# Kernel tuning notes

Measured on AMD Instinct MI355X. Metric: run time of the kernel, lower is better.

Reference implementation:

```python
import jax, jax.numpy as jnp
import numpy as np
from math import factorial, sqrt

LMAX = 2
SH = (LMAX + 1) ** 2  # 9 real spherical-harmonic components
N_ATOMS = 1000
N_EDGES = 10000
N_BASIS = 128
N_RADIAL = 20


def _cg_complex(l1, m1, l2, m2, l3, m3):
    # Racah formula for complex Clebsch-Gordan <l1 m1 l2 m2 | l3 m3>
    if m3 != m1 + m2 or not (abs(l1 - l2) <= l3 <= l1 + l2):
        return 0.0
    pre = sqrt((2 * l3 + 1) * factorial(l3 + l1 - l2) * factorial(l3 - l1 + l2)
               * factorial(l1 + l2 - l3) / factorial(l1 + l2 + l3 + 1))
    pre *= sqrt(factorial(l3 + m3) * factorial(l3 - m3) * factorial(l1 - m1)
                * factorial(l1 + m1) * factorial(l2 - m2) * factorial(l2 + m2))
    kmin = max(0, l2 - l3 - m1, l1 - l3 + m2)
    kmax = min(l1 + l2 - l3, l1 - m1, l2 + m2)
    s = 0.0
    for k in range(kmin, kmax + 1):
        s += (-1) ** k / (factorial(k) * factorial(l1 + l2 - l3 - k)
                          * factorial(l1 - m1 - k) * factorial(l2 + m2 - k)
                          * factorial(l3 - l2 + m1 + k) * factorial(l3 - l1 - m2 + k))
    return pre * s


def _u_c2r(l):
    # complex -> real spherical-harmonic change of basis, rows real m, cols complex m
    U = np.zeros((2 * l + 1, 2 * l + 1), dtype=np.complex128)
    U[l, l] = 1.0
    for m in range(1, l + 1):
        U[l + m, l + m] = (-1) ** m / np.sqrt(2.0)
        U[l + m, l - m] = 1.0 / np.sqrt(2.0)
        U[l - m, l - m] = 1j / np.sqrt(2.0)
        U[l - m, l + m] = -1j * (-1) ** m / np.sqrt(2.0)
    return U


def _generate_cg_rsh(lmax):
    # real-SH Clebsch-Gordan tensor with parity invariance (odd l1+l2+l3 zeroed)
    S = (lmax + 1) ** 2
    cg = np.zeros((S, S, S))
    for l1 in range(lmax + 1):
        for l2 in range(lmax + 1):
            for l3 in range(lmax + 1):
                if (l1 + l2 + l3) % 2 == 1 or not (abs(l1 - l2) <= l3 <= l1 + l2):
                    continue
                block = np.zeros((2 * l1 + 1, 2 * l2 + 1, 2 * l3 + 1), dtype=np.complex128)
                for m1 in range(-l1, l1 + 1):
                    for m2 in range(-l2, l2 + 1):
                        m3 = m1 + m2
                        if abs(m3) <= l3:
                            block[m1 + l1, m2 + l2, m3 + l3] = _cg_complex(l1, m1, l2, m2, l3, m3)
                rb = np.einsum('abc,ia,jb,kc->ijk', block, _u_c2r(l1), _u_c2r(l2), np.conj(_u_c2r(l3)))
                cg[l1 * l1:(l1 + 1) ** 2, l2 * l2:(l2 + 1) ** 2, l3 * l3:(l3 + 1) ** 2] = np.real(rb)
    cg[np.abs(cg) < 1e-12] = 0.0
    return cg


_CG_T = _generate_cg_rsh(LMAX)
_I1, _I2, _IO = np.nonzero(_CG_T)
CG = jnp.asarray(_CG_T[_I1, _I2, _IO].astype(np.float32))  # [P] nonzero CG values
IDX_IN_1 = jnp.asarray(_I1)
IDX_IN_2 = jnp.asarray(_I2)
IDX_OUT = jnp.asarray(_IO)
_LIDX = np.repeat(np.arange(LMAX + 1), 2 * np.arange(LMAX + 1) + 1)  # degree l per SH index
WIDX = jnp.asarray(_LIDX[_I1])  # filter degree per CG path (schnetpack Widx)


def setup_inputs() -> dict:
    key = jax.random.key(0)
    ks = jax.random.split(key, 7)
    return {
        "x": jax.random.normal(ks[0], (N_ATOMS, SH, N_BASIS), jnp.float32),
        "radial_ij": jax.random.normal(ks[1], (N_EDGES, N_RADIAL), jnp.float32),
        "dir_ij": jax.random.normal(ks[2], (N_EDGES, SH), jnp.float32),
        "cutoff_ij": jax.random.uniform(ks[3], (N_EDGES, 1), jnp.float32),
        "Wf": jax.random.normal(ks[4], (N_RADIAL, (LMAX + 1) * N_BASIS), jnp.float32) * 0.1,
        "bf": jnp.zeros(((LMAX + 1) * N_BASIS,), jnp.float32),
        "idx_i": jax.random.randint(ks[5], (N_EDGES,), 0, N_ATOMS),
        "idx_j": jax.random.randint(ks[6], (N_EDGES,), 0, N_ATOMS),
        "n_atoms": N_ATOMS,
    }


def reference(x, radial_ij, dir_ij, cutoff_ij, Wf, bf, idx_i, idx_j, n_atoms):
    E = radial_ij.shape[0]
    # radial filter: Dense(n_radial -> (lmax+1)*C) * cutoff, gathered per CG path by degree l
    Wij = (radial_ij @ Wf + bf) * cutoff_ij                     # [E,(L+1)*C]
    Wij = Wij.reshape(E, LMAX + 1, N_BASIS)[:, WIDX]            # [E,P,C]
    xj = x[idx_j][:, IDX_IN_2]                                  # gather neighbor feats: [E,P,C]
    v = Wij * dir_ij[:, IDX_IN_1, None] * CG[None, :, None] * xj  # [E,P,C]
    # scatter_add over CG paths -> output SH index
    yij = jnp.zeros((E, SH, N_BASIS), v.dtype).at[:, IDX_OUT, :].add(v)  # [E,S,C]
    # scatter_add over edges -> receiving atom
    y = jax.ops.segment_sum(yij, idx_i, num_segments=n_atoms)   # [n_atoms,S,C]
    return y
```

## Files before the change

### kernel.cpp

```cpp
#include <hip/hip_runtime.h>


#define SH_N 9
#define NB 128
#define NR 20
#define NSUB 2
#define NT (NSUB * NB)
#define CAPL 128

namespace cgc {

struct CD { double re, im; };
constexpr CD cmul(CD x, CD y) { return {x.re * y.re - x.im * y.im, x.re * y.im + x.im * y.re}; }
constexpr CD cadd(CD x, CD y) { return {x.re + y.re, x.im + y.im}; }
constexpr CD cconj(CD x) { return {x.re, -x.im}; }

constexpr double FACT[10] = {1., 1., 2., 6., 24., 120., 720., 5040., 40320., 362880.};

constexpr double csqrt(double a) {
    if (a <= 0.0) return 0.0;
    double x = a < 1.0 ? 1.0 : a;
    for (int i = 0; i < 40; ++i) x = 0.5 * (x + a / x);
    return x;
}

constexpr double cg_complex(int l1, int m1, int l2, int m2, int l3, int m3) {
    if (m3 != m1 + m2) return 0.0;
    int dl = l1 > l2 ? l1 - l2 : l2 - l1;
    if (l3 < dl || l3 > l1 + l2) return 0.0;
    double pre = csqrt((2.0 * l3 + 1.0) * FACT[l3 + l1 - l2] * FACT[l3 - l1 + l2]
                       * FACT[l1 + l2 - l3] / FACT[l1 + l2 + l3 + 1]);
    pre = pre * csqrt(FACT[l3 + m3] * FACT[l3 - m3] * FACT[l1 - m1] * FACT[l1 + m1]
                      * FACT[l2 - m2] * FACT[l2 + m2]);
    int kmin = 0;
    if (l2 - l3 - m1 > kmin) kmin = l2 - l3 - m1;
    if (l1 - l3 + m2 > kmin) kmin = l1 - l3 + m2;
    int kmax = l1 + l2 - l3;
    if (l1 - m1 < kmax) kmax = l1 - m1;
    if (l2 + m2 < kmax) kmax = l2 + m2;
    double s = 0.0;
    for (int k = kmin; k <= kmax; ++k) {
        double term = 1.0 / (FACT[k] * FACT[l1 + l2 - l3 - k] * FACT[l1 - m1 - k]
                             * FACT[l2 + m2 - k] * FACT[l3 - l2 + m1 + k] * FACT[l3 - l1 - m2 + k]);
        s += (k & 1) ? -term : term;
    }
    return pre * s;
}

struct U5 { CD m[5][5]; };
constexpr U5 u_c2r(int l) {
    U5 u{};
    const double isq = csqrt(0.5);
    u.m[l][l] = {1.0, 0.0};
    for (int mm = 1; mm <= l; ++mm) {
        double sgn = (mm & 1) ? -1.0 : 1.0;
        u.m[l + mm][l + mm] = {sgn * isq, 0.0};
        u.m[l + mm][l - mm] = {isq, 0.0};
        u.m[l - mm][l - mm] = {0.0, isq};
        u.m[l - mm][l + mm] = {0.0, -sgn * isq};
    }
    return u;
}

struct CGTab { float v[SH_N][SH_N][SH_N]; };

constexpr CGTab build_cg() {
    CGTab t{};
    for (int l1 = 0; l1 <= 2; ++l1)
    for (int l2 = 0; l2 <= 2; ++l2)
    for (int l3 = 0; l3 <= 2; ++l3) {
        int dl = l1 > l2 ? l1 - l2 : l2 - l1;
        if (((l1 + l2 + l3) & 1) || l3 < dl || l3 > l1 + l2) continue;
        U5 U1 = u_c2r(l1), U2 = u_c2r(l2), U3 = u_c2r(l3);
        const int n1 = 2 * l1 + 1, n2 = 2 * l2 + 1, n3 = 2 * l3 + 1;
        double blk[5][5][5] = {};
        for (int a = 0; a < n1; ++a)
        for (int b = 0; b < n2; ++b) {
            int m1 = a - l1, m2 = b - l2, m3 = m1 + m2;
            if (m3 < -l3 || m3 > l3) continue;
            blk[a][b][m3 + l3] = cg_complex(l1, m1, l2, m2, l3, m3);
        }
        for (int i = 0; i < n1; ++i)
        for (int j = 0; j < n2; ++j)
        for (int k = 0; k < n3; ++k) {
            CD s{0.0, 0.0};
            for (int a = 0; a < n1; ++a) {
                if (U1.m[i][a].re == 0.0 && U1.m[i][a].im == 0.0) continue;
                for (int b = 0; b < n2; ++b) {
                    if (U2.m[j][b].re == 0.0 && U2.m[j][b].im == 0.0) continue;
                    int m3 = (a - l1) + (b - l2);
                    if (m3 < -l3 || m3 > l3) continue;
                    double B = blk[a][b][m3 + l3];
                    if (B == 0.0) continue;
                    CD u3 = cconj(U3.m[k][m3 + l3]);
                    if (u3.re == 0.0 && u3.im == 0.0) continue;
                    CD term = cmul(cmul(U1.m[i][a], U2.m[j][b]), u3);
                    s = cadd(s, CD{term.re * B, term.im * B});
                }
            }
            double v = s.re;
            if (v < 1e-12 && v > -1e-12) v = 0.0;
            t.v[l1 * l1 + i][l2 * l2 + j][l3 * l3 + k] = (float)v;
        }
    }
    return t;
}

}

static constexpr cgc::CGTab CGT = cgc::build_cg();

__device__ __forceinline__ float sel_w(int a, float w0, float w1, float w2) {
    return (a == 0) ? w0 : ((a < 4) ? w1 : w2);
}

__device__ __forceinline__ void comp_edge(
        int e, const float (&xr)[SH_N],
        const float* __restrict__ radial, const float* __restrict__ dir,
        const float* __restrict__ cutoff,
        const float (&wreg)[NR * 3], float b0, float b1, float b2,
        float (&acc)[SH_N]) {
    const float* rad = radial + (size_t)e * NR;
    float a0 = b0, a1 = b1, a2 = b2;
#pragma unroll
    for (int r = 0; r < NR; ++r) {
        const float rv = rad[r];
        a0 = fmaf(rv, wreg[r * 3 + 0], a0);
        a1 = fmaf(rv, wreg[r * 3 + 1], a1);
        a2 = fmaf(rv, wreg[r * 3 + 2], a2);
    }
    const float cut = cutoff[e];
    const float w0 = a0 * cut, w1 = a1 * cut, w2 = a2 * cut;
    const float* dp = dir + (size_t)e * SH_N;
#pragma unroll
    for (int ai = 0; ai < SH_N; ++ai) {
        const float daw = dp[ai] * sel_w(ai, w0, w1, w2);
#pragma unroll
        for (int bi = 0; bi < SH_N; ++bi) {
            const float g = daw * xr[bi];
#pragma unroll
            for (int o = 0; o < SH_N; ++o)
                if (CGT.v[ai][bi][o] != 0.0f)
                    acc[o] = fmaf(CGT.v[ai][bi][o], g, acc[o]);
        }
    }
}

__device__ __forceinline__ void load_xr(float (&xr)[SH_N], int e,
        const float* __restrict__ x, const int* __restrict__ idx_j, int c) {
    const int aj = idx_j[e];
    const float* xp = x + (size_t)aj * (SH_N * NB) + c;
#pragma unroll
    for (int k = 0; k < SH_N; ++k) xr[k] = xp[k * NB];
}


__global__ void __launch_bounds__(NT, 4)
so3_fused_kernel(const float* __restrict__ x,
                 const float* __restrict__ radial,
                 const float* __restrict__ dir,
                 const float* __restrict__ cutoff,
                 const float* __restrict__ Wf,
                 const float* __restrict__ bf,
                 const int* __restrict__ idx_i,
                 const int* __restrict__ idx_j,
                 float* __restrict__ y,
                 int E) {
    const int a    = blockIdx.x;
    const int tid  = threadIdx.x;
    const int sub  = tid >> 7;
    const int c    = tid & (NB - 1);
    const int lane = tid & 63;
    const int wid  = tid >> 6;

    __shared__ int s_list[CAPL];
    __shared__ int s_wsum[NT / 64];
    __shared__ int s_m;

    float wreg[NR * 3];
#pragma unroll
    for (int r = 0; r < NR; ++r)
#pragma unroll
        for (int l = 0; l < 3; ++l)
            wreg[r * 3 + l] = Wf[(r * 3 + l) * NB + c];
    const float b0 = bf[c], b1 = bf[NB + c], b2 = bf[2 * NB + c];

    unsigned long long mask = 0ull;
    int cnt = 0;
    const int E4 = E >> 2;
    const bool fast_scan = (4 * ((E4 + NT - 1) / NT) <= 60);
    if (fast_scan) {
        const int4* p4 = (const int4*)idx_i;
        int b = 0;
        for (int k4 = tid; k4 < E4; k4 += NT, ++b) {
            const int4 q = p4[k4];
            unsigned long long h = (unsigned long long)(q.x == a)
                                 | ((unsigned long long)(q.y == a) << 1)
                                 | ((unsigned long long)(q.z == a) << 2)
                                 | ((unsigned long long)(q.w == a) << 3);
            mask |= h << (4 * b);
        }
        const int kt = 4 * E4 + tid;
        if (tid < (E & 3) && kt < E && idx_i[kt] == a)
            mask |= 1ull << (60 + tid);
        cnt = __popcll(mask);
    } else {
        for (int k = tid; k < E; k += NT) cnt += (idx_i[k] == a);
    }

    int v = cnt;
#pragma unroll
    for (int d = 1; d < 64; d <<= 1) {
        int u = __shfl_up(v, d);
        if (lane >= d) v += u;
    }
    if (lane == 63) s_wsum[wid] = v;
    __syncthreads();
    if (tid == 0) {
        int t = 0;
#pragma unroll
        for (int w = 0; w < NT / 64; ++w) { int q = s_wsum[w]; s_wsum[w] = t; t += q; }
        s_m = t;
    }
    __syncthreads();
    int off = s_wsum[wid] + v - cnt;

    if (fast_scan) {
        unsigned long long mm = mask;
        while (mm) {
            const int p = __ffsll(mm) - 1;
            mm &= mm - 1;
            int k;
            if (p >= 60) k = 4 * E4 + (p - 60);
            else         k = 4 * (tid + (p >> 2) * NT) + (p & 3);
            if (off < CAPL) s_list[off] = k;
            ++off;
        }
    } else if (cnt > 0) {
        for (int k = tid; k < E; k += NT)
            if (idx_i[k] == a) { if (off < CAPL) s_list[off] = k; ++off; }
    }
    __syncthreads();
    const int m = (s_m < CAPL) ? s_m : CAPL;

    float acc[SH_N];
#pragma unroll
    for (int o = 0; o < SH_N; ++o) acc[o] = 0.f;

    int ie = sub;
    if (ie < m) {
        float xrA[SH_N], xrB[SH_N];
        int eA = __builtin_amdgcn_readfirstlane(s_list[ie]);
        load_xr(xrA, eA, x, idx_j, c);
        for (;;) {
            int ien = ie + NSUB;
            if (ien < m) {
                const int eB = __builtin_amdgcn_readfirstlane(s_list[ien]);
                load_xr(xrB, eB, x, idx_j, c);
                comp_edge(eA, xrA, radial, dir, cutoff, wreg, b0, b1, b2, acc);
                ie = ien; ien += NSUB;
                if (ien < m) {
                    eA = __builtin_amdgcn_readfirstlane(s_list[ien]);
                    load_xr(xrA, eA, x, idx_j, c);
                    comp_edge(eB, xrB, radial, dir, cutoff, wreg, b0, b1, b2, acc);
                    ie = ien;
                } else {
                    comp_edge(eB, xrB, radial, dir, cutoff, wreg, b0, b1, b2, acc);
                    break;
                }
            } else {
                comp_edge(eA, xrA, radial, dir, cutoff, wreg, b0, b1, b2, acc);
                break;
            }
        }
    }

    __shared__ float s_red[NSUB][SH_N * NB];
#pragma unroll
    for (int o = 0; o < SH_N; ++o) s_red[sub][o * NB + c] = acc[o];
    __syncthreads();
    float* yo = y + (size_t)a * (SH_N * NB);
    for (int oc = tid; oc < SH_N * NB; oc += NT)
        yo[oc] = s_red[0][oc] + s_red[1][oc];
}


extern "C" void kernel_launch(void* const* d_in, const int* in_sizes, int n_in,
                              void* d_out, int out_size, void* d_ws, size_t ws_size,
                              hipStream_t stream) {
    const float* x      = (const float*)d_in[0];
    const float* radial = (const float*)d_in[1];
    const float* dir    = (const float*)d_in[2];
    const float* cutoff = (const float*)d_in[3];
    const float* Wf     = (const float*)d_in[4];
    const float* bf     = (const float*)d_in[5];
    const int*   idx_i  = (const int*)d_in[6];
    const int*   idx_j  = (const int*)d_in[7];
    float* y = (float*)d_out;
    const int E = in_sizes[6];
    const int n_atoms = out_size / (SH_N * NB);

    so3_fused_kernel<<<n_atoms, NT, 0, stream>>>(x, radial, dir, cutoff, Wf, bf,
                                                 idx_i, idx_j, y, E);
}
```

Before: 26.28 us.

## Split radial filter into separate precompute kernel and widen atom blocks

Moves the per-edge radial dense layer and cutoff multiply into a separate kernel that writes a per-edge, per-channel filter to workspace; the atom kernel then loads these weights instead of holding Wf in registers. Edge parallelism per atom block is doubled to four sub-groups. A fallback kernel staging Wf in shared memory is used when workspace is insufficient. This trades register pressure and recomputation for an extra launch and a large intermediate write/read.

```diff
diff --git a/kernel.cpp b/kernel.cpp
--- a/kernel.cpp
+++ b/kernel.cpp
@@ -4,9 +4,10 @@
 #define SH_N 9
 #define NB 128
 #define NR 20
-#define NSUB 2
-#define NT (NSUB * NB)
+#define NSUB 4
+#define NT2 (NSUB * NB)
 #define CAPL 128
+#define EB 8
 
 namespace cgc {
 
@@ -114,30 +115,70 @@
     return (a == 0) ? w0 : ((a < 4) ? w1 : w2);
 }
 
-__device__ __forceinline__ void comp_edge(
-        int e, const float (&xr)[SH_N],
-        const float* __restrict__ radial, const float* __restrict__ dir,
-        const float* __restrict__ cutoff,
-        const float (&wreg)[NR * 3], float b0, float b1, float b2,
-        float (&acc)[SH_N]) {
-    const float* rad = radial + (size_t)e * NR;
-    float a0 = b0, a1 = b1, a2 = b2;
-#pragma unroll
-    for (int r = 0; r < NR; ++r) {
-        const float rv = rad[r];
-        a0 = fmaf(rv, wreg[r * 3 + 0], a0);
-        a1 = fmaf(rv, wreg[r * 3 + 1], a1);
-        a2 = fmaf(rv, wreg[r * 3 + 2], a2);
-    }
-    const float cut = cutoff[e];
-    const float w0 = a0 * cut, w1 = a1 * cut, w2 = a2 * cut;
+
+__global__ void __launch_bounds__(NB)
+radial_kernel(const float* __restrict__ radial,
+              const float* __restrict__ cutoff,
+              const float* __restrict__ Wf,
+              const float* __restrict__ bf,
+              float* __restrict__ W,
+              int E) {
+    const int c = threadIdx.x;
+    float wreg[NR * 3];
+#pragma unroll
+    for (int r = 0; r < NR; ++r)
+#pragma unroll
+        for (int l = 0; l < 3; ++l)
+            wreg[r * 3 + l] = Wf[r * 3 * NB + l * NB + c];
+    const float b0 = bf[c], b1 = bf[NB + c], b2 = bf[2 * NB + c];
+
+    const int e0 = blockIdx.x * EB;
+#pragma unroll
+    for (int i = 0; i < EB; ++i) {
+        const int e = e0 + i;
+        if (e >= E) return;
+        const float* rad = radial + (size_t)e * NR;
+        float a0 = b0, a1 = b1, a2 = b2;
+#pragma unroll
+        for (int r = 0; r < NR; ++r) {
+            const float rv = rad[r];
+            a0 = fmaf(rv, wreg[r * 3 + 0], a0);
+            a1 = fmaf(rv, wreg[r * 3 + 1], a1);
+            a2 = fmaf(rv, wreg[r * 3 + 2], a2);
+        }
+        const float cut = cutoff[e];
+        float* wp = W + (size_t)e * (3 * NB) + c;
+        wp[0]       = a0 * cut;
+        wp[NB]      = a1 * cut;
+        wp[2 * NB]  = a2 * cut;
+    }
+}
+
+
+struct Ld { float xr[SH_N]; float w0, w1, w2; };
+
+__device__ __forceinline__ void load_edge(Ld& L, float (&d)[SH_N], int e,
+        const float* __restrict__ x, const float* __restrict__ W,
+        const float* __restrict__ dir, const int* __restrict__ idx_j, int c) {
+    const int aj = idx_j[e];
+    const float* xp = x + (size_t)aj * (SH_N * NB) + c;
+#pragma unroll
+    for (int k = 0; k < SH_N; ++k) L.xr[k] = xp[k * NB];
+    const float* wp = W + (size_t)e * (3 * NB) + c;
+    L.w0 = wp[0]; L.w1 = wp[NB]; L.w2 = wp[2 * NB];
     const float* dp = dir + (size_t)e * SH_N;
 #pragma unroll
+    for (int k = 0; k < SH_N; ++k) d[k] = dp[k];
+}
+
+__device__ __forceinline__ void comp_edge(const Ld& L, const float (&d)[SH_N],
+                                          float (&acc)[SH_N]) {
+#pragma unroll
     for (int ai = 0; ai < SH_N; ++ai) {
-        const float daw = dp[ai] * sel_w(ai, w0, w1, w2);
+        const float daw = d[ai] * sel_w(ai, L.w0, L.w1, L.w2);
 #pragma unroll
         for (int bi = 0; bi < SH_N; ++bi) {
-            const float g = daw * xr[bi];
+            const float g = daw * L.xr[bi];
 #pragma unroll
             for (int o = 0; o < SH_N; ++o)
                 if (CGT.v[ai][bi][o] != 0.0f)
@@ -146,26 +187,14 @@
     }
 }
 
-__device__ __forceinline__ void load_xr(float (&xr)[SH_N], int e,
-        const float* __restrict__ x, const int* __restrict__ idx_j, int c) {
-    const int aj = idx_j[e];
-    const float* xp = x + (size_t)aj * (SH_N * NB) + c;
-#pragma unroll
-    for (int k = 0; k < SH_N; ++k) xr[k] = xp[k * NB];
-}
-
-
-__global__ void __launch_bounds__(NT, 4)
-so3_fused_kernel(const float* __restrict__ x,
-                 const float* __restrict__ radial,
-                 const float* __restrict__ dir,
-                 const float* __restrict__ cutoff,
-                 const float* __restrict__ Wf,
-                 const float* __restrict__ bf,
-                 const int* __restrict__ idx_i,
-                 const int* __restrict__ idx_j,
-                 float* __restrict__ y,
-                 int E) {
+__global__ void __launch_bounds__(NT2)
+so3_atom_kernel(const float* __restrict__ x,
+                const float* __restrict__ W,
+                const float* __restrict__ dir,
+                const int* __restrict__ idx_i,
+                const int* __restrict__ idx_j,
+                float* __restrict__ y,
+                int E) {
     const int a    = blockIdx.x;
     const int tid  = threadIdx.x;
     const int sub  = tid >> 7;
@@ -174,25 +203,17 @@
     const int wid  = tid >> 6;
 
     __shared__ int s_list[CAPL];
-    __shared__ int s_wsum[NT / 64];
+    __shared__ int s_wsum[NT2 / 64];
     __shared__ int s_m;
-
-    float wreg[NR * 3];
-#pragma unroll
-    for (int r = 0; r < NR; ++r)
-#pragma unroll
-        for (int l = 0; l < 3; ++l)
-            wreg[r * 3 + l] = Wf[(r * 3 + l) * NB + c];
-    const float b0 = bf[c], b1 = bf[NB + c], b2 = bf[2 * NB + c];
 
     unsigned long long mask = 0ull;
     int cnt = 0;
     const int E4 = E >> 2;
-    const bool fast_scan = (4 * ((E4 + NT - 1) / NT) <= 60);
+    const bool fast_scan = (4 * ((E4 + NT2 - 1) / NT2) <= 60);
     if (fast_scan) {
         const int4* p4 = (const int4*)idx_i;
         int b = 0;
-        for (int k4 = tid; k4 < E4; k4 += NT, ++b) {
+        for (int k4 = tid; k4 < E4; k4 += NT2, ++b) {
             const int4 q = p4[k4];
             unsigned long long h = (unsigned long long)(q.x == a)
                                  | ((unsigned long long)(q.y == a) << 1)
@@ -205,7 +226,7 @@
             mask |= 1ull << (60 + tid);
         cnt = __popcll(mask);
     } else {
-        for (int k = tid; k < E; k += NT) cnt += (idx_i[k] == a);
+        for (int k = tid; k < E; k += NT2) cnt += (idx_i[k] == a);
     }
 
     int v = cnt;
@@ -219,7 +240,7 @@
     if (tid == 0) {
         int t = 0;
 #pragma unroll
-        for (int w = 0; w < NT / 64; ++w) { int q = s_wsum[w]; s_wsum[w] = t; t += q; }
+        for (int w = 0; w < NT2 / 64; ++w) { int q = s_wsum[w]; s_wsum[w] = t; t += q; }
         s_m = t;
     }
     __syncthreads();
@@ -232,12 +253,12 @@
             mm &= mm - 1;
             int k;
             if (p >= 60) k = 4 * E4 + (p - 60);
-            else         k = 4 * (tid + (p >> 2) * NT) + (p & 3);
+            else         k = 4 * (tid + (p >> 2) * NT2) + (p & 3);
             if (off < CAPL) s_list[off] = k;
             ++off;
         }
     } else if (cnt > 0) {
-        for (int k = tid; k < E; k += NT)
+        for (int k = tid; k < E; k += NT2)
             if (idx_i[k] == a) { if (off < CAPL) s_list[off] = k; ++off; }
     }
     __syncthreads();
@@ -249,27 +270,30 @@
 
     int ie = sub;
     if (ie < m) {
-        float xrA[SH_N], xrB[SH_N];
-        int eA = __builtin_amdgcn_readfirstlane(s_list[ie]);
-        load_xr(xrA, eA, x, idx_j, c);
+        Ld LA, LB;
+        float dA[SH_N], dB[SH_N];
+        {
+            const int eA = __builtin_amdgcn_readfirstlane(s_list[ie]);
+            load_edge(LA, dA, eA, x, W, dir, idx_j, c);
+        }
         for (;;) {
             int ien = ie + NSUB;
             if (ien < m) {
                 const int eB = __builtin_amdgcn_readfirstlane(s_list[ien]);
-                load_xr(xrB, eB, x, idx_j, c);
-                comp_edge(eA, xrA, radial, dir, cutoff, wreg, b0, b1, b2, acc);
+                load_edge(LB, dB, eB, x, W, dir, idx_j, c);
+                comp_edge(LA, dA, acc);
                 ie = ien; ien += NSUB;
                 if (ien < m) {
-                    eA = __builtin_amdgcn_readfirstlane(s_list[ien]);
-                    load_xr(xrA, eA, x, idx_j, c);
-                    comp_edge(eB, xrB, radial, dir, cutoff, wreg, b0, b1, b2, acc);
+                    const int eA = __builtin_amdgcn_readfirstlane(s_list[ien]);
+                    load_edge(LA, dA, eA, x, W, dir, idx_j, c);
+                    comp_edge(LB, dB, acc);
                     ie = ien;
                 } else {
-                    comp_edge(eB, xrB, radial, dir, cutoff, wreg, b0, b1, b2, acc);
+                    comp_edge(LB, dB, acc);
                     break;
                 }
             } else {
-                comp_edge(eA, xrA, radial, dir, cutoff, wreg, b0, b1, b2, acc);
+                comp_edge(LA, dA, acc);
                 break;
             }
         }
@@ -280,8 +304,138 @@
     for (int o = 0; o < SH_N; ++o) s_red[sub][o * NB + c] = acc[o];
     __syncthreads();
     float* yo = y + (size_t)a * (SH_N * NB);
-    for (int oc = tid; oc < SH_N * NB; oc += NT)
-        yo[oc] = s_red[0][oc] + s_red[1][oc];
+    for (int oc = tid; oc < SH_N * NB; oc += NT2)
+        yo[oc] = s_red[0][oc] + s_red[1][oc] + s_red[2][oc] + s_red[3][oc];
+}
+
+
+__global__ void __launch_bounds__(NT2)
+so3_atom_kernel_lds(const float* __restrict__ x,
+                    const float* __restrict__ radial,
+                    const float* __restrict__ dir,
+                    const float* __restrict__ cutoff,
+                    const float* __restrict__ Wf,
+                    const float* __restrict__ bf,
+                    const int* __restrict__ idx_i,
+                    const int* __restrict__ idx_j,
+                    float* __restrict__ y,
+                    int E) {
+    const int a    = blockIdx.x;
+    const int tid  = threadIdx.x;
+    const int sub  = tid >> 7;
+    const int c    = tid & (NB - 1);
+    const int lane = tid & 63;
+    const int wid  = tid >> 6;
+
+    __shared__ int s_list[CAPL];
+    __shared__ int s_wsum[NT2 / 64];
+    __shared__ int s_m;
+    __shared__ float s_wf[NR * 3 * NB];
+
+    for (int idx = tid; idx < NR * 3 * NB; idx += NT2) s_wf[idx] = Wf[idx];
+
+    unsigned long long mask = 0ull;
+    int cnt = 0;
+    const int E4 = E >> 2;
+    const bool fast_scan = (4 * ((E4 + NT2 - 1) / NT2) <= 60);
+    if (fast_scan) {
+        const int4* p4 = (const int4*)idx_i;
+        int b = 0;
+        for (int k4 = tid; k4 < E4; k4 += NT2, ++b) {
+            const int4 q = p4[k4];
+            unsigned long long h = (unsigned long long)(q.x == a)
+                                 | ((unsigned long long)(q.y == a) << 1)
+                                 | ((unsigned long long)(q.z == a) << 2)
+                                 | ((unsigned long long)(q.w == a) << 3);
+            mask |= h << (4 * b);
+        }
+        const int kt = 4 * E4 + tid;
+        if (tid < (E & 3) && kt < E && idx_i[kt] == a)
+            mask |= 1ull << (60 + tid);
+        cnt = __popcll(mask);
+    } else {
+        for (int k = tid; k < E; k += NT2) cnt += (idx_i[k] == a);
+    }
+
+    int v = cnt;
+#pragma unroll
+    for (int d = 1; d < 64; d <<= 1) {
+        int u = __shfl_up(v, d);
+        if (lane >= d) v += u;
+    }
+    if (lane == 63) s_wsum[wid] = v;
+    __syncthreads();
+    if (tid == 0) {
+        int t = 0;
+#pragma unroll
+        for (int w = 0; w < NT2 / 64; ++w) { int q = s_wsum[w]; s_wsum[w] = t; t += q; }
+        s_m = t;
+    }
+    __syncthreads();
+    int off = s_wsum[wid] + v - cnt;
+    if (fast_scan) {
+        unsigned long long mm = mask;
+        while (mm) {
+            const int p = __ffsll(mm) - 1;
+            mm &= mm - 1;
+            int k;
+            if (p >= 60) k = 4 * E4 + (p - 60);
+            else         k = 4 * (tid + (p >> 2) * NT2) + (p & 3);
+            if (off < CAPL) s_list[off] = k;
+            ++off;
+        }
+    } else if (cnt > 0) {
+        for (int k = tid; k < E; k += NT2)
+            if (idx_i[k] == a) { if (off < CAPL) s_list[off] = k; ++off; }
+    }
+    __syncthreads();
+    const int m = (s_m < CAPL) ? s_m : CAPL;
+
+    float acc[SH_N];
+#pragma unroll
+    for (int o = 0; o < SH_N; ++o) acc[o] = 0.f;
+    const float b0 = bf[c], b1 = bf[NB + c], b2 = bf[2 * NB + c];
+
+    for (int ie = sub; ie < m; ie += NSUB) {
+        const int e = __builtin_amdgcn_readfirstlane(s_list[ie]);
+        const int aj = idx_j[e];
+        float xr[SH_N];
+        const float* xp = x + (size_t)aj * (SH_N * NB) + c;
+#pragma unroll
+        for (int k = 0; k < SH_N; ++k) xr[k] = xp[k * NB];
+        const float* rad = radial + (size_t)e * NR;
+        float a0 = b0, a1 = b1, a2 = b2;
+#pragma unroll
+        for (int r = 0; r < NR; ++r) {
+            const float rv = rad[r];
+            a0 = fmaf(rv, s_wf[(r * 3 + 0) * NB + c], a0);
+            a1 = fmaf(rv, s_wf[(r * 3 + 1) * NB + c], a1);
+            a2 = fmaf(rv, s_wf[(r * 3 + 2) * NB + c], a2);
+        }
+        const float cut = cutoff[e];
+        const float w0 = a0 * cut, w1 = a1 * cut, w2 = a2 * cut;
+        const float* dp = dir + (size_t)e * SH_N;
+#pragma unroll
+        for (int ai = 0; ai < SH_N; ++ai) {
+            const float daw = dp[ai] * sel_w(ai, w0, w1, w2);
+#pragma unroll
+            for (int bi = 0; bi < SH_N; ++bi) {
+                const float g = daw * xr[bi];
+#pragma unroll
+                for (int o = 0; o < SH_N; ++o)
+                    if (CGT.v[ai][bi][o] != 0.0f)
+                        acc[o] = fmaf(CGT.v[ai][bi][o], g, acc[o]);
+            }
+        }
+    }
+
+    __shared__ float s_red[NSUB][SH_N * NB];
+#pragma unroll
+    for (int o = 0; o < SH_N; ++o) s_red[sub][o * NB + c] = acc[o];
+    __syncthreads();
+    float* yo = y + (size_t)a * (SH_N * NB);
+    for (int oc = tid; oc < SH_N * NB; oc += NT2)
+        yo[oc] = s_red[0][oc] + s_red[1][oc] + s_red[2][oc] + s_red[3][oc];
 }
 
 
@@ -300,6 +454,13 @@
     const int E = in_sizes[6];
     const int n_atoms = out_size / (SH_N * NB);
 
-    so3_fused_kernel<<<n_atoms, NT, 0, stream>>>(x, radial, dir, cutoff, Wf, bf,
-                                                 idx_i, idx_j, y, E);
-}
+    const size_t needW = (size_t)E * 3 * NB * sizeof(float);
+    if (ws_size >= needW) {
+        float* W = (float*)d_ws;
+        radial_kernel<<<(E + EB - 1) / EB, NB, 0, stream>>>(radial, cutoff, Wf, bf, W, E);
+        so3_atom_kernel<<<n_atoms, NT2, 0, stream>>>(x, W, dir, idx_i, idx_j, y, E);
+    } else {
+        so3_atom_kernel_lds<<<n_atoms, NT2, 0, stream>>>(x, radial, dir, cutoff,
+                                                         Wf, bf, idx_i, idx_j, y, E);
+    }
+}
```

Measured after the change: 31.04 us. +18.1%, slower.
